# Performance work log

Measured on AMD Instinct MI355X. Metric: run time of the kernel, lower is better.

Reference implementation:

```python
import jax, jax.numpy as jnp
import numpy as np

N = 50000      # nodes
E = 800000     # edges
G = 64         # graphs in batch
DIN = 128
H = 128
DOUT = 128
EPS = 1e-5     # BatchNorm eps
SLOPE = 0.01   # leaky_relu negative slope


def setup_inputs() -> dict:
    key = jax.random.key(0)
    ks = jax.random.split(key, 12)
    x = jax.random.normal(ks[0], (N, DIN), jnp.float32)
    edge_index = jax.random.randint(ks[1], (2, E), 0, N)
    batch = jnp.sort(jax.random.randint(ks[2], (N,), 0, G))
    edge_weight = jax.random.uniform(ks[3], (E,), jnp.float32)

    def lin(k, i, o):
        return (jax.random.normal(k, (i, o), jnp.float32) / np.float32(np.sqrt(i)))

    W0, b0 = lin(ks[4], DIN, H), jnp.zeros((H,), jnp.float32)
    W1, b1 = lin(ks[5], H, H), jnp.zeros((H,), jnp.float32)
    W2, b2 = lin(ks[6], H, DOUT), jnp.zeros((DOUT,), jnp.float32)
    # BatchNorm (eval mode): affine params + running stats
    g0, be0 = jnp.ones((H,), jnp.float32), jnp.zeros((H,), jnp.float32)
    m0 = 0.1 * jax.random.normal(ks[7], (H,), jnp.float32)
    v0 = jax.random.uniform(ks[8], (H,), jnp.float32, minval=0.5, maxval=1.5)
    g1, be1 = jnp.ones((H,), jnp.float32), jnp.zeros((H,), jnp.float32)
    m1 = 0.1 * jax.random.normal(ks[9], (H,), jnp.float32)
    v1 = jax.random.uniform(ks[10], (H,), jnp.float32, minval=0.5, maxval=1.5)
    return dict(x=x, edge_weight=edge_weight, W0=W0, b0=b0, W1=W1, b1=b1,
                W2=W2, b2=b2, g0=g0, be0=be0, m0=m0, v0=v0,
                g1=g1, be1=be1, m1=m1, v1=v1,
                edge_index=edge_index, batch=batch)


def _gcn_conv(x, src, dst, w, W, b):
    # PyG GCNConv: x' = D^{-1/2}(A + I)D^{-1/2} (x W) + b, self-loop weight 1.
    x = x @ W                                   # [N, out]
    deg = jax.ops.segment_sum(w, dst, num_segments=N)          # [N]
    safe = jnp.where(deg > 0, deg, 1.0)
    dinv = jnp.where(deg > 0, 1.0 / jnp.sqrt(safe), 0.0)        # deg^{-1/2}, inf->0
    norm = dinv[src] * w * dinv[dst]                             # [E+N]
    msgs = x[src] * norm[:, None]                                # [E+N, out]
    return jax.ops.segment_sum(msgs, dst, num_segments=N) + b


def _bn_eval(x, g, b, m, v):
    return (x - m) * jax.lax.rsqrt(v + EPS) * g + b


def _leaky(x):
    return jnp.where(x > 0, x, SLOPE * x)


def reference(x, edge_weight, W0, b0, W1, b1, W2, b2,
              g0, be0, m0, v0, g1, be1, m1, v1, edge_index, batch):
    loops = jnp.arange(N)
    src = jnp.concatenate([edge_index[0], loops])
    dst = jnp.concatenate([edge_index[1], loops])
    w = jnp.concatenate([edge_weight, jnp.ones((N,), edge_weight.dtype)])

    h = _leaky(_bn_eval(_gcn_conv(x, src, dst, w, W0, b0), g0, be0, m0, v0))
    h = _leaky(_bn_eval(_gcn_conv(h, src, dst, w, W1, b1), g1, be1, m1, v1))
    h = _gcn_conv(h, src, dst, w, W2, b2)                        # [N, DOUT]

    # global_mean_pool over batch assignment
    sums = jax.ops.segment_sum(h, batch, num_segments=G)         # [G, DOUT]
    cnt = jax.ops.segment_sum(jnp.ones((N,), h.dtype), batch, num_segments=G)
    return sums / jnp.clip(cnt, 1.0)[:, None]
```

## Files before the change

kernel.cpp:

```cpp
#include <hip/hip_runtime.h>

#define EPS 1e-5f
#define SLOPE 0.01f
#define FIXP 262144.0f
#define RSTRIDE 64

typedef short short8 __attribute__((ext_vector_type(8)));
typedef float f32x4 __attribute__((ext_vector_type(4)));
typedef float f32x2 __attribute__((ext_vector_type(2)));

static __device__ __forceinline__ unsigned short f32_to_bf16(float x){
  unsigned int u = __float_as_uint(x);
  unsigned int r = u + 0x7FFFu + ((u >> 16) & 1u);
  return (unsigned short)(r >> 16);
}
static __device__ __forceinline__ float bf16lo_to_f32(unsigned int v){
  return __uint_as_float(v << 16);
}
static __device__ __forceinline__ float bf16hi_to_f32(unsigned int v){
  return __uint_as_float(v & 0xFFFF0000u);
}


__global__ void k_packzero(const float* __restrict__ W0, const float* __restrict__ W1,
                           const float* __restrict__ W2, short* __restrict__ Bh,
                           short* __restrict__ Bl, unsigned int* __restrict__ cnt,
                           int n){
  if ((int)blockIdx.x >= 192){
    int idx = ((int)blockIdx.x - 192)*256 + threadIdx.x;
    if (idx < n) cnt[idx] = 0u;
    return;
  }
  int idx = blockIdx.x*256 + threadIdx.x;
  int which = idx >> 14;
  int r = idx & 16383;
  const float* W = (which == 0) ? W0 : ((which == 1) ? W1 : W2);
  int j = r & 7;
  int l = (r >> 3) & 63;
  int s = (r >> 9) & 3;
  int t = r >> 11;
  int k = s*32 + ((l >> 4) << 3) + j;
  int nn = t*16 + (l & 15);
  float v = W[k*128 + nn];
  unsigned short hb = f32_to_bf16(v);
  float hf = bf16lo_to_f32(hb);
  unsigned short lb = f32_to_bf16(v - hf);
  Bh[idx] = (short)hb;
  Bl[idx] = (short)lb;
}


__global__ __launch_bounds__(256) void k_fused0(
    const int* __restrict__ dst, const float* __restrict__ ew,
    unsigned int* __restrict__ cnt, int* __restrict__ pwr, int E, int GB,
    const float* __restrict__ X, const short* __restrict__ Bh,
    const short* __restrict__ Bl, unsigned short* __restrict__ Y, int nrows){
  int bid = (int)blockIdx.x;
  if (bid >= GB){
    int e = (bid - GB)*256 + (int)threadIdx.x;
    if (e < E){
      unsigned int add = (1u << 24) | (unsigned int)(ew[e] * FIXP);
      unsigned int old = atomicAdd(&cnt[dst[e]], add);
      pwr[e] = (int)(old >> 24);
    }
    return;
  }
  int w    = threadIdx.x >> 6;
  int lane = threadIdx.x & 63;
  int m    = lane & 15;
  int kg   = lane >> 4;
  int row0 = bid*64 + w*16;

  f32x4 acc[8];
  #pragma unroll
  for (int t = 0; t < 8; ++t) acc[t] = (f32x4){0.f, 0.f, 0.f, 0.f};

  int arow = row0 + m;
  if (arow >= nrows) arow = nrows - 1;
  const float* ap0 = X + (size_t)arow*128 + (kg << 3);
  const short8* bh0 = (const short8*)Bh + lane;
  const short8* bl0 = (const short8*)Bl + lane;

  #pragma unroll
  for (int s = 0; s < 4; ++s){
    const float* ap = ap0 + s*32;
    float4 a0 = *(const float4*)ap;
    float4 a1 = *(const float4*)(ap + 4);
    float av[8] = {a0.x, a0.y, a0.z, a0.w, a1.x, a1.y, a1.z, a1.w};
    short8 ah, al;
    #pragma unroll
    for (int j = 0; j < 8; ++j){
      unsigned short hb = f32_to_bf16(av[j]);
      float hf = bf16lo_to_f32(hb);
      ah[j] = (short)hb;
      al[j] = (short)f32_to_bf16(av[j] - hf);
    }
    #pragma unroll
    for (int t = 0; t < 8; ++t){
      short8 bh = bh0[t*256 + s*64];
      short8 bl = bl0[t*256 + s*64];
      acc[t] = __builtin_amdgcn_mfma_f32_16x16x32_bf16(ah, bh, acc[t], 0, 0, 0);
      acc[t] = __builtin_amdgcn_mfma_f32_16x16x32_bf16(al, bh, acc[t], 0, 0, 0);
      acc[t] = __builtin_amdgcn_mfma_f32_16x16x32_bf16(ah, bl, acc[t], 0, 0, 0);
    }
  }
  #pragma unroll
  for (int t = 0; t < 8; ++t){
    #pragma unroll
    for (int r = 0; r < 4; ++r){
      int grow = row0 + (kg << 2) + r;
      if (grow < nrows) Y[(size_t)grow*128 + t*16 + m] = f32_to_bf16(acc[t][r]);
    }
  }
}


__global__ void k_fill(const int* __restrict__ src, const int* __restrict__ dst,
                       const float* __restrict__ w, const int* __restrict__ pwr,
                       const unsigned int* __restrict__ cnt,
                       int2* __restrict__ csr, int E){
  int e = blockIdx.x*blockDim.x + threadIdx.x;
  if (e >= E) return;
  int d = dst[e], s = src[e];
  int slot = pwr[e];
  unsigned int cd = cnt[d], cs = cnt[s];
  float dgd = 1.0f + (float)(cd & 0xFFFFFFu) * (1.0f/FIXP);
  float dgs = 1.0f + (float)(cs & 0xFFFFFFu) * (1.0f/FIXP);
  float nr = rsqrtf(dgd) * rsqrtf(dgs) * w[e];
  if (slot < RSTRIDE)
    csr[((size_t)d << 6) + slot] = make_int2(s, __float_as_int(nr));
}


#define ACC4(v, nn) \
  acc[0] += (f32x2){bf16lo_to_f32((v).x), bf16hi_to_f32((v).x)} * (nn); \
  acc[1] += (f32x2){bf16lo_to_f32((v).y), bf16hi_to_f32((v).y)} * (nn); \
  acc[2] += (f32x2){bf16lo_to_f32((v).z), bf16hi_to_f32((v).z)} * (nn); \
  acc[3] += (f32x2){bf16lo_to_f32((v).w), bf16hi_to_f32((v).w)} * (nn);

template<bool BN>
__global__ __launch_bounds__(256) void k_gather(
    const unsigned short* __restrict__ Y, const unsigned int* __restrict__ cnt,
    const int2* __restrict__ csr,
    const float* __restrict__ bias,
    const float* __restrict__ gam, const float* __restrict__ bet,
    const float* __restrict__ mean, const float* __restrict__ var,
    unsigned int* __restrict__ outv, int n){
  int wid  = (blockIdx.x * blockDim.x + threadIdx.x) >> 6;
  int lane = threadIdx.x & 63;
  if (wid >= n) return;
  int g = lane >> 4;
  int q = lane & 15;

  unsigned int cw = cnt[wid];
  int len = (int)(cw >> 24);
  if (len > RSTRIDE) len = RSTRIDE;

  int cex = 0, cey = 0;
  if (lane < len){
    int2 ce = csr[((size_t)wid << 6) + lane];
    cex = ce.x; cey = ce.y;
  }

  f32x2 acc[4];
  #pragma unroll
  for (int j = 0; j < 4; ++j) acc[j] = (f32x2){0.f, 0.f};

  const char* Yb = (const char*)Y;

  for (int base = 0; base < len; base += 16){
    #pragma unroll
    for (int u = 0; u < 4; ++u){
      int j = base + g*4 + u;
      bool valid = j < len;
      int sj = __shfl(cex, j, 64);
      int nj = __shfl(cey, j, 64);
      unsigned su = valid ? (unsigned)sj : 0u;
      float nr = valid ? __int_as_float(nj) : 0.f;
      uint4 v = *(const uint4*)(Yb + ((size_t)su << 8) + (q << 4));
      ACC4(v, nr);
    }
  }

  float s[8] = {acc[0].x, acc[0].y, acc[1].x, acc[1].y,
                acc[2].x, acc[2].y, acc[3].x, acc[3].y};
  #pragma unroll
  for (int j = 0; j < 8; ++j){
    s[j] += __shfl_xor(s[j], 16, 64);
    s[j] += __shfl_xor(s[j], 32, 64);
  }

  float t[8];
  int srcl = lane >> 2;
  #pragma unroll
  for (int j = 0; j < 8; ++j) t[j] = __shfl(s[j], srcl, 64);
  float a0 = (lane & 1) ? t[2] : t[0];
  float a1 = (lane & 1) ? t[3] : t[1];
  float b0 = (lane & 1) ? t[6] : t[4];
  float b1 = (lane & 1) ? t[7] : t[5];
  float o0 = (lane & 2) ? b0 : a0;
  float o1 = (lane & 2) ? b1 : a1;

  unsigned int sv = *(const unsigned int*)(Yb + ((size_t)wid << 8) + (lane << 2));
  float dg = 1.0f + (float)(cw & 0xFFFFFFu) * (1.0f/FIXP);
  float sf = 1.0f / dg;
  o0 += bf16lo_to_f32(sv) * sf;
  o1 += bf16hi_to_f32(sv) * sf;

  int c = lane << 1;
  float2 bi = *(const float2*)&bias[c];
  o0 += bi.x; o1 += bi.y;
  if (BN){
    float2 ga = *(const float2*)&gam[c];
    float2 bt = *(const float2*)&bet[c];
    float2 mn = *(const float2*)&mean[c];
    float2 vr = *(const float2*)&var[c];
    float ax = ga.x * rsqrtf(vr.x + EPS);
    float ay = ga.y * rsqrtf(vr.y + EPS);
    o0 = (o0 - mn.x) * ax + bt.x;
    o1 = (o1 - mn.y) * ay + bt.y;
    o0 = o0 > 0.f ? o0 : SLOPE*o0;
    o1 = o1 > 0.f ? o1 : SLOPE*o1;
  }
  unsigned int pk = ((unsigned int)f32_to_bf16(o1) << 16) | f32_to_bf16(o0);
  outv[((size_t)wid << 6) + lane] = pk;
}


__global__ __launch_bounds__(256) void k_gemm_bf16(const unsigned short* __restrict__ Xb,
                                                   const short* __restrict__ Bh,
                                                   const short* __restrict__ Bl,
                                                   unsigned short* __restrict__ Y,
                                                   int nrows){
  int w    = threadIdx.x >> 6;
  int lane = threadIdx.x & 63;
  int m    = lane & 15;
  int kg   = lane >> 4;
  int row0 = blockIdx.x*64 + w*16;

  f32x4 acc[8];
  #pragma unroll
  for (int t = 0; t < 8; ++t) acc[t] = (f32x4){0.f, 0.f, 0.f, 0.f};

  int arow = row0 + m;
  if (arow >= nrows) arow = nrows - 1;
  const short8* ap = (const short8*)(Xb + (size_t)arow*128) + kg;
  const short8* bh0 = (const short8*)Bh + lane;
  const short8* bl0 = (const short8*)Bl + lane;

  #pragma unroll
  for (int s = 0; s < 4; ++s){
    short8 a = ap[s*4];
    #pragma unroll
    for (int t = 0; t < 8; ++t){
      acc[t] = __builtin_amdgcn_mfma_f32_16x16x32_bf16(a, bh0[t*256 + s*64], acc[t], 0, 0, 0);
      acc[t] = __builtin_amdgcn_mfma_f32_16x16x32_bf16(a, bl0[t*256 + s*64], acc[t], 0, 0, 0);
    }
  }
  #pragma unroll
  for (int t = 0; t < 8; ++t){
    #pragma unroll
    for (int r = 0; r < 4; ++r){
      int grow = row0 + (kg << 2) + r;
      if (grow < nrows) Y[(size_t)grow*128 + t*16 + m] = f32_to_bf16(acc[t][r]);
    }
  }
}


__global__ void k_pool(const unsigned int* __restrict__ h, const int* __restrict__ batch,
                       float* __restrict__ out, int n){
  __shared__ float2 red[1024];
  __shared__ int ss[2];
  int g = blockIdx.x;
  if (threadIdx.x < 2){
    int target = g + (int)threadIdx.x;
    int lo = 0, hi = n;
    while (lo < hi){ int mid = (lo + hi) >> 1; if (batch[mid] < target) lo = mid + 1; else hi = mid; }
    ss[threadIdx.x] = lo;
  }
  __syncthreads();
  int a = ss[0], b = ss[1];
  int rg = threadIdx.x >> 6;
  int c2 = threadIdx.x & 63;
  float sx = 0.f, sy = 0.f;
  for (int i = a + rg; i < b; i += 16){
    unsigned int v = h[((size_t)i << 6) + c2];
    sx += bf16lo_to_f32(v);
    sy += bf16hi_to_f32(v);
  }
  red[threadIdx.x] = make_float2(sx, sy);
  __syncthreads();
  if (rg == 0){
    float tx = 0.f, ty = 0.f;
    #pragma unroll
    for (int k = 0; k < 16; ++k){
      float2 r = red[c2 + k*64];
      tx += r.x; ty += r.y;
    }
    int cn = b - a;
    float inv = 1.0f / (float)(cn > 0 ? cn : 1);
    out[g*128 + 2*c2]     = tx * inv;
    out[g*128 + 2*c2 + 1] = ty * inv;
  }
}


extern "C" void kernel_launch(void* const* d_in, const int* in_sizes, int n_in,
                              void* d_out, int out_size, void* d_ws, size_t ws_size,
                              hipStream_t stream) {
  const int N = in_sizes[0] / 128;
  const int E = in_sizes[1];
  const int G = out_size / 128;
  const int NB = (N + 255) / 256;
  const int CB = (E + 255) / 256;
  const int GB = (N + 63) / 64;

  const float* x   = (const float*)d_in[0];
  const float* ew  = (const float*)d_in[1];
  const float* W0  = (const float*)d_in[2];
  const float* b0  = (const float*)d_in[3];
  const float* W1  = (const float*)d_in[4];
  const float* b1  = (const float*)d_in[5];
  const float* W2  = (const float*)d_in[6];
  const float* b2  = (const float*)d_in[7];
  const float* g0  = (const float*)d_in[8];
  const float* be0 = (const float*)d_in[9];
  const float* m0  = (const float*)d_in[10];
  const float* v0  = (const float*)d_in[11];
  const float* g1  = (const float*)d_in[12];
  const float* be1 = (const float*)d_in[13];
  const float* m1  = (const float*)d_in[14];
  const float* v1  = (const float*)d_in[15];
  const int*   ei  = (const int*)d_in[16];
  const int*   bat = (const int*)d_in[17];
  float* out = (float*)d_out;

  char* p = (char*)d_ws;
  auto alloc = [&](size_t bytes)->char*{
    char* q = p; p += (bytes + 255) & ~(size_t)255; return q;
  };
  unsigned int* cnt = (unsigned int*)alloc((size_t)N*4);
  int*   pwr    = (int*)  alloc((size_t)E*4);
  int2*  csr    = (int2*) alloc((size_t)N*RSTRIDE*8);
  unsigned short* Y  = (unsigned short*)alloc((size_t)N*128*2);
  unsigned short* Hb = (unsigned short*)alloc((size_t)N*128*2);
  short* Bh = (short*)alloc(3*16384*2);
  short* Bl = (short*)alloc(3*16384*2);

  const int* src = ei;
  const int* dst = ei + E;

  k_packzero<<<192 + NB, 256, 0, stream>>>(W0, W1, W2, Bh, Bl, cnt, N);
  k_fused0<<<GB + CB, 256, 0, stream>>>(dst, ew, cnt, pwr, E, GB, x, Bh, Bl, Y, N);
  k_fill  <<<CB, 256, 0, stream>>>(src, dst, ew, pwr, cnt, csr, E);

  k_gather<true><<<(N+3)/4, 256, 0, stream>>>(Y, cnt, csr,
                                              b0, g0, be0, m0, v0, (unsigned int*)Hb, N);
  k_gemm_bf16<<<GB, 256, 0, stream>>>(Hb, Bh + 16384, Bl + 16384, Y, N);
  k_gather<true><<<(N+3)/4, 256, 0, stream>>>(Y, cnt, csr,
                                              b1, g1, be1, m1, v1, (unsigned int*)Hb, N);
  k_gemm_bf16<<<GB, 256, 0, stream>>>(Hb, Bh + 32768, Bl + 32768, Y, N);
  k_gather<false><<<(N+3)/4, 256, 0, stream>>>(Y, cnt, csr,
                                               b2, nullptr, nullptr, nullptr, nullptr,
                                               (unsigned int*)Hb, N);
  k_pool<<<G, 1024, 0, stream>>>((const unsigned int*)Hb, bat, out, N);
}
```

Baseline: 218.1 us.

## Fuse final GCN gather with mean-pool via per-block shared partial sums

The last-layer gather now accumulates each node's output directly into shared-memory per-graph slots (up to 8 graphs per 16-node block), writes per-block partials, and a small second kernel sums the partials per graph. This removes the write and re-read of the full bf16 final hidden matrix and the bf16 rounding before pooling. It adds shared-memory atomics and a 1024-thread block shape. Correctness relies on sorted batch ids and at most 8 distinct graphs per block.

```diff
diff --git a/kernel.cpp b/kernel.cpp
--- a/kernel.cpp
+++ b/kernel.cpp
@@ -131,14 +131,78 @@
     csr[((size_t)d << 6) + slot] = make_int2(s, __float_as_int(nr));
 }
 
-
 #define ACC4(v, nn) \
   acc[0] += (f32x2){bf16lo_to_f32((v).x), bf16hi_to_f32((v).x)} * (nn); \
   acc[1] += (f32x2){bf16lo_to_f32((v).y), bf16hi_to_f32((v).y)} * (nn); \
   acc[2] += (f32x2){bf16lo_to_f32((v).z), bf16hi_to_f32((v).z)} * (nn); \
   acc[3] += (f32x2){bf16lo_to_f32((v).w), bf16hi_to_f32((v).w)} * (nn);
 
-template<bool BN>
+static __device__ __forceinline__ void gather_core(
+    const unsigned short* __restrict__ Y, const int2* __restrict__ csr,
+    const float* __restrict__ bias, unsigned int cw, int wid, int lane,
+    float& o0, float& o1){
+  int g = lane >> 4;
+  int q = lane & 15;
+  int len = (int)(cw >> 24);
+  if (len > RSTRIDE) len = RSTRIDE;
+
+  int cex = 0, cey = 0;
+  if (lane < len){
+    int2 ce = csr[((size_t)wid << 6) + lane];
+    cex = ce.x; cey = ce.y;
+  }
+
+  f32x2 acc[4];
+  #pragma unroll
+  for (int j = 0; j < 4; ++j) acc[j] = (f32x2){0.f, 0.f};
+
+  const char* Yb = (const char*)Y;
+
+  for (int base = 0; base < len; base += 16){
+    #pragma unroll
+    for (int u = 0; u < 4; ++u){
+      int j = base + g*4 + u;
+      bool valid = j < len;
+      int sj = __shfl(cex, j, 64);
+      int nj = __shfl(cey, j, 64);
+      unsigned su = valid ? (unsigned)sj : 0u;
+      float nr = valid ? __int_as_float(nj) : 0.f;
+      uint4 v = *(const uint4*)(Yb + ((size_t)su << 8) + (q << 4));
+      ACC4(v, nr);
+    }
+  }
+
+  float s[8] = {acc[0].x, acc[0].y, acc[1].x, acc[1].y,
+                acc[2].x, acc[2].y, acc[3].x, acc[3].y};
+  #pragma unroll
+  for (int j = 0; j < 8; ++j){
+    s[j] += __shfl_xor(s[j], 16, 64);
+    s[j] += __shfl_xor(s[j], 32, 64);
+  }
+
+  float t[8];
+  int srcl = lane >> 2;
+  #pragma unroll
+  for (int j = 0; j < 8; ++j) t[j] = __shfl(s[j], srcl, 64);
+  float a0 = (lane & 1) ? t[2] : t[0];
+  float a1 = (lane & 1) ? t[3] : t[1];
+  float b0 = (lane & 1) ? t[6] : t[4];
+  float b1 = (lane & 1) ? t[7] : t[5];
+  o0 = (lane & 2) ? b0 : a0;
+  o1 = (lane & 2) ? b1 : a1;
+
+  unsigned int sv = *(const unsigned int*)(Yb + ((size_t)wid << 8) + (lane << 2));
+  float dg = 1.0f + (float)(cw & 0xFFFFFFu) * (1.0f/FIXP);
+  float sf = 1.0f / dg;
+  o0 += bf16lo_to_f32(sv) * sf;
+  o1 += bf16hi_to_f32(sv) * sf;
+
+  int c = lane << 1;
+  float2 bi = *(const float2*)&bias[c];
+  o0 += bi.x; o1 += bi.y;
+}
+
+
 __global__ __launch_bounds__(256) void k_gather(
     const unsigned short* __restrict__ Y, const unsigned int* __restrict__ cnt,
     const int2* __restrict__ csr,
@@ -149,81 +213,82 @@
   int wid  = (blockIdx.x * blockDim.x + threadIdx.x) >> 6;
   int lane = threadIdx.x & 63;
   if (wid >= n) return;
-  int g = lane >> 4;
-  int q = lane & 15;
-
-  unsigned int cw = cnt[wid];
-  int len = (int)(cw >> 24);
-  if (len > RSTRIDE) len = RSTRIDE;
-
-  int cex = 0, cey = 0;
-  if (lane < len){
-    int2 ce = csr[((size_t)wid << 6) + lane];
-    cex = ce.x; cey = ce.y;
-  }
-
-  f32x2 acc[4];
-  #pragma unroll
-  for (int j = 0; j < 4; ++j) acc[j] = (f32x2){0.f, 0.f};
-
-  const char* Yb = (const char*)Y;
-
-  for (int base = 0; base < len; base += 16){
-    #pragma unroll
-    for (int u = 0; u < 4; ++u){
-      int j = base + g*4 + u;
-      bool valid = j < len;
-      int sj = __shfl(cex, j, 64);
-      int nj = __shfl(cey, j, 64);
-      unsigned su = valid ? (unsigned)sj : 0u;
-      float nr = valid ? __int_as_float(nj) : 0.f;
-      uint4 v = *(const uint4*)(Yb + ((size_t)su << 8) + (q << 4));
-      ACC4(v, nr);
-    }
-  }
-
-  float s[8] = {acc[0].x, acc[0].y, acc[1].x, acc[1].y,
-                acc[2].x, acc[2].y, acc[3].x, acc[3].y};
-  #pragma unroll
-  for (int j = 0; j < 8; ++j){
-    s[j] += __shfl_xor(s[j], 16, 64);
-    s[j] += __shfl_xor(s[j], 32, 64);
-  }
-
-  float t[8];
-  int srcl = lane >> 2;
-  #pragma unroll
-  for (int j = 0; j < 8; ++j) t[j] = __shfl(s[j], srcl, 64);
-  float a0 = (lane & 1) ? t[2] : t[0];
-  float a1 = (lane & 1) ? t[3] : t[1];
-  float b0 = (lane & 1) ? t[6] : t[4];
-  float b1 = (lane & 1) ? t[7] : t[5];
-  float o0 = (lane & 2) ? b0 : a0;
-  float o1 = (lane & 2) ? b1 : a1;
-
-  unsigned int sv = *(const unsigned int*)(Yb + ((size_t)wid << 8) + (lane << 2));
-  float dg = 1.0f + (float)(cw & 0xFFFFFFu) * (1.0f/FIXP);
-  float sf = 1.0f / dg;
-  o0 += bf16lo_to_f32(sv) * sf;
-  o1 += bf16hi_to_f32(sv) * sf;
+
+  float o0, o1;
+  gather_core(Y, csr, bias, cnt[wid], wid, lane, o0, o1);
 
   int c = lane << 1;
-  float2 bi = *(const float2*)&bias[c];
-  o0 += bi.x; o1 += bi.y;
-  if (BN){
-    float2 ga = *(const float2*)&gam[c];
-    float2 bt = *(const float2*)&bet[c];
-    float2 mn = *(const float2*)&mean[c];
-    float2 vr = *(const float2*)&var[c];
-    float ax = ga.x * rsqrtf(vr.x + EPS);
-    float ay = ga.y * rsqrtf(vr.y + EPS);
-    o0 = (o0 - mn.x) * ax + bt.x;
-    o1 = (o1 - mn.y) * ay + bt.y;
-    o0 = o0 > 0.f ? o0 : SLOPE*o0;
-    o1 = o1 > 0.f ? o1 : SLOPE*o1;
-  }
+  float2 ga = *(const float2*)&gam[c];
+  float2 bt = *(const float2*)&bet[c];
+  float2 mn = *(const float2*)&mean[c];
+  float2 vr = *(const float2*)&var[c];
+  float ax = ga.x * rsqrtf(vr.x + EPS);
+  float ay = ga.y * rsqrtf(vr.y + EPS);
+  o0 = (o0 - mn.x) * ax + bt.x;
+  o1 = (o1 - mn.y) * ay + bt.y;
+  o0 = o0 > 0.f ? o0 : SLOPE*o0;
+  o1 = o1 > 0.f ? o1 : SLOPE*o1;
+
   unsigned int pk = ((unsigned int)f32_to_bf16(o1) << 16) | f32_to_bf16(o0);
   outv[((size_t)wid << 6) + lane] = pk;
+}
+
+
+__global__ __launch_bounds__(1024) void k_gatherpool(
+    const unsigned short* __restrict__ Y, const unsigned int* __restrict__ cnt,
+    const int2* __restrict__ csr, const float* __restrict__ bias,
+    const int* __restrict__ batch, float* __restrict__ partial, int n){
+  __shared__ float accum[8][128];
+  __shared__ int s_gfirst;
+  int w    = threadIdx.x >> 6;
+  int lane = threadIdx.x & 63;
+  if (threadIdx.x < 1024) ((float*)accum)[threadIdx.x] = 0.f;
+  if (threadIdx.x == 0) s_gfirst = batch[blockIdx.x*16];
+  __syncthreads();
+
+  int node = blockIdx.x*16 + w;
+  if (node < n){
+    float o0, o1;
+    gather_core(Y, csr, bias, cnt[node], node, lane, o0, o1);
+    int gid = batch[node];
+    int slot = gid - s_gfirst;
+    if (slot > 7) slot = 7;
+    atomicAdd(&accum[slot][lane*2],     o0);
+    atomicAdd(&accum[slot][lane*2 + 1], o1);
+  }
+  __syncthreads();
+  int slot = threadIdx.x >> 7;
+  int c    = threadIdx.x & 127;
+  partial[((size_t)blockIdx.x*8 + slot)*128 + c] = accum[slot][c];
+}
+
+
+__global__ __launch_bounds__(128) void k_pool2(
+    const float* __restrict__ partial, const int* __restrict__ batch,
+    float* __restrict__ out, int n, int gnum){
+  __shared__ int ss[2];
+  int g = blockIdx.x;
+  if (threadIdx.x < 2){
+    int target = g + (int)threadIdx.x;
+    int lo = 0, hi = n;
+    while (lo < hi){ int mid = (lo + hi) >> 1; if (batch[mid] < target) lo = mid + 1; else hi = mid; }
+    ss[threadIdx.x] = lo;
+  }
+  __syncthreads();
+  int a = ss[0], b = ss[1];
+  int c = threadIdx.x;
+  float s = 0.f;
+  if (b > a){
+    int B0 = a >> 4, B1 = (b - 1) >> 4;
+    for (int B = B0; B <= B1; ++B){
+      int gf = batch[B*16];
+      int slot = g - gf;
+      if (slot >= 0 && slot < 8)
+        s += partial[((size_t)B*8 + slot)*128 + c];
+    }
+  }
+  int cn = b - a;
+  out[g*128 + c] = s / (float)(cn > 0 ? cn : 1);
 }
 
 
@@ -268,44 +333,6 @@
 }
 
 
-__global__ void k_pool(const unsigned int* __restrict__ h, const int* __restrict__ batch,
-                       float* __restrict__ out, int n){
-  __shared__ float2 red[1024];
-  __shared__ int ss[2];
-  int g = blockIdx.x;
-  if (threadIdx.x < 2){
-    int target = g + (int)threadIdx.x;
-    int lo = 0, hi = n;
-    while (lo < hi){ int mid = (lo + hi) >> 1; if (batch[mid] < target) lo = mid + 1; else hi = mid; }
-    ss[threadIdx.x] = lo;
-  }
-  __syncthreads();
-  int a = ss[0], b = ss[1];
-  int rg = threadIdx.x >> 6;
-  int c2 = threadIdx.x & 63;
-  float sx = 0.f, sy = 0.f;
-  for (int i = a + rg; i < b; i += 16){
-    unsigned int v = h[((size_t)i << 6) + c2];
-    sx += bf16lo_to_f32(v);
-    sy += bf16hi_to_f32(v);
-  }
-  red[threadIdx.x] = make_float2(sx, sy);
-  __syncthreads();
-  if (rg == 0){
-    float tx = 0.f, ty = 0.f;
-    #pragma unroll
-    for (int k = 0; k < 16; ++k){
-      float2 r = red[c2 + k*64];
-      tx += r.x; ty += r.y;
-    }
-    int cn = b - a;
-    float inv = 1.0f / (float)(cn > 0 ? cn : 1);
-    out[g*128 + 2*c2]     = tx * inv;
-    out[g*128 + 2*c2 + 1] = ty * inv;
-  }
-}
-
-
 extern "C" void kernel_launch(void* const* d_in, const int* in_sizes, int n_in,
                               void* d_out, int out_size, void* d_ws, size_t ws_size,
                               hipStream_t stream) {
@@ -315,6 +342,7 @@
   const int NB = (N + 255) / 256;
   const int CB = (E + 255) / 256;
   const int GB = (N + 63) / 64;
+  const int PB = (N + 15) / 16;
 
   const float* x   = (const float*)d_in[0];
   const float* ew  = (const float*)d_in[1];
@@ -345,6 +373,7 @@
   int2*  csr    = (int2*) alloc((size_t)N*RSTRIDE*8);
   unsigned short* Y  = (unsigned short*)alloc((size_t)N*128*2);
   unsigned short* Hb = (unsigned short*)alloc((size_t)N*128*2);
+  float* partial = (float*)alloc((size_t)PB*8*128*4);
   short* Bh = (short*)alloc(3*16384*2);
   short* Bl = (short*)alloc(3*16384*2);
 
@@ -355,14 +384,12 @@
   k_fused0<<<GB + CB, 256, 0, stream>>>(dst, ew, cnt, pwr, E, GB, x, Bh, Bl, Y, N);
   k_fill  <<<CB, 256, 0, stream>>>(src, dst, ew, pwr, cnt, csr, E);
 
-  k_gather<true><<<(N+3)/4, 256, 0, stream>>>(Y, cnt, csr,
-                                              b0, g0, be0, m0, v0, (unsigned int*)Hb, N);
+  k_gather<<<(N+3)/4, 256, 0, stream>>>(Y, cnt, csr,
+                                        b0, g0, be0, m0, v0, (unsigned int*)Hb, N);
   k_gemm_bf16<<<GB, 256, 0, stream>>>(Hb, Bh + 16384, Bl + 16384, Y, N);
-  k_gather<true><<<(N+3)/4, 256, 0, stream>>>(Y, cnt, csr,
-                                              b1, g1, be1, m1, v1, (unsigned int*)Hb, N);
+  k_gather<<<(N+3)/4, 256, 0, stream>>>(Y, cnt, csr,
+                                        b1, g1, be1, m1, v1, (unsigned int*)Hb, N);
   k_gemm_bf16<<<GB, 256, 0, stream>>>(Hb, Bh + 32768, Bl + 32768, Y, N);
-  k_gather<false><<<(N+3)/4, 256, 0, stream>>>(Y, cnt, csr,
-                                               b2, nullptr, nullptr, nullptr, nullptr,
-                                               (unsigned int*)Hb, N);
-  k_pool<<<G, 1024, 0, stream>>>((const unsigned int*)Hb, bat, out, N);
-}
+  k_gatherpool<<<PB, 1024, 0, stream>>>(Y, cnt, csr, b2, bat, partial, N);
+  k_pool2<<<G, 128, 0, stream>>>(partial, bat, out, N, G);
+}
```

After: 259.7 us. 19.1% more time.
